# Kernel tuning notes

Hardware: AMD Instinct MI355X
Metric: run time of the kernel (lower is better)

## Reference

```python
import jax, jax.numpy as jnp
import numpy as np

BATCH, SEQ, IN, HID, LAYERS = 128, 512, 512, 1024, 2


def setup_inputs() -> dict:
    key = jax.random.key(0)
    ks = jax.random.split(key, 8)
    s = 0.02
    # Gate weights concatenated in order [forget, input, output, cell]
    W0 = jax.random.normal(ks[0], (IN + HID, 4 * HID), dtype=jnp.float32) * s
    b0 = jax.random.normal(ks[1], (4 * HID,), dtype=jnp.float32) * s
    W1 = jax.random.normal(ks[2], (HID + HID, 4 * HID), dtype=jnp.float32) * s
    b1 = jax.random.normal(ks[3], (4 * HID,), dtype=jnp.float32) * s
    Wout = jax.random.normal(ks[4], (HID, 1), dtype=jnp.float32) * s
    bout = jax.random.normal(ks[5], (1,), dtype=jnp.float32) * s
    x = jax.random.normal(ks[6], (BATCH, SEQ, IN), dtype=jnp.float32)
    return {"x": x, "W0": W0, "b0": b0, "W1": W1, "b1": b1,
            "Wout": Wout, "bout": bout}


def _cell(x_in, h_prev, c_prev, W, b):
    z = jnp.concatenate([x_in, h_prev], axis=-1) @ W + b  # (B, 4H)
    f, i, o, g = jnp.split(z, 4, axis=-1)
    c_next = jax.nn.sigmoid(f) * c_prev + jax.nn.sigmoid(i) * jnp.tanh(g)
    h_next = jax.nn.sigmoid(o) * jnp.tanh(c_next)
    return h_next, c_next


def reference(x, W0, b0, W1, b1, Wout, bout):
    B = x.shape[0]
    H = W0.shape[1] // 4
    params = ((W0, b0), (W1, b1))

    h0 = tuple(jnp.zeros((B, H), x.dtype) for _ in range(LAYERS))
    c0 = tuple(jnp.zeros((B, H), x.dtype) for _ in range(LAYERS))

    def step(carry, x_t):
        h, c = carry
        inp = x_t
        new_h, new_c = [], []
        for l in range(LAYERS):
            W, b = params[l]
            h_n, c_n = _cell(inp, h[l], c[l], W, b)
            new_h.append(h_n)
            new_c.append(c_n)
            inp = h_n
        return (tuple(new_h), tuple(new_c)), None

    xs = jnp.swapaxes(x, 0, 1)  # (T, B, IN)
    (h_fin, _), _ = jax.lax.scan(step, (h0, c0), xs)
    last = h_fin[-1]  # output of top layer at last timestep
    logits = last @ Wout + bout  # (B, 1)
    return jax.nn.sigmoid(logits).squeeze(-1)  # (B,)
```

## Files before the change

kernel.cpp:

```cpp
#include <hip/hip_runtime.h>
#include <hip/hip_bf16.h>
#include <cstdint>
#include <cstddef>


#define BATCH 128
#define SEQ   512
#define INP   512
#define HID   1024
#define NCOL  4096
#define NB    256
#define KS0   48
#define KS1   64
#define HS_   (BATCH * HID)

typedef __bf16 bf16x8 __attribute__((ext_vector_type(8)));
typedef float  f32x4  __attribute__((ext_vector_type(4)));
typedef unsigned int u32x4 __attribute__((ext_vector_type(4)));
typedef unsigned long long u64;
typedef u64 u64x2 __attribute__((ext_vector_type(2)));

__device__ __forceinline__ bf16x8 load_bf16x8(const __hip_bfloat16* p) {
    u32x4 u = *reinterpret_cast<const u32x4*>(p);
    return __builtin_bit_cast(bf16x8, u);
}
__device__ __forceinline__ bf16x8 aload_bf16x8(const __hip_bfloat16* p) {
    u64x2 q;
    q[0] = __hip_atomic_load((const u64*)p,       __ATOMIC_RELAXED, __HIP_MEMORY_SCOPE_AGENT);
    q[1] = __hip_atomic_load((const u64*)(p + 4), __ATOMIC_RELAXED, __HIP_MEMORY_SCOPE_AGENT);
    return __builtin_bit_cast(bf16x8, q);
}
__device__ __forceinline__ f32x4 mfma16(bf16x8 a, bf16x8 b, f32x4 c) {
    return __builtin_amdgcn_mfma_f32_16x16x32_bf16(a, b, c, 0, 0, 0);
}
__device__ __forceinline__ float sigmoidf_(float x) {
    return 1.0f / (1.0f + __expf(-x));
}
__device__ __forceinline__ float tanhf_(float x) {
    return 1.0f - 2.0f / (__expf(2.0f * x) + 1.0f);
}
__device__ __forceinline__ void gload16(const void* g, void* l) {
    __builtin_amdgcn_global_load_lds(
        (const __attribute__((address_space(1))) uint32_t*)g,
        (__attribute__((address_space(3))) uint32_t*)l, 16, 0, 0);
}
#define VMWAIT asm volatile("s_waitcnt vmcnt(12)" ::: "memory")

template<int Ks>
__global__ __launch_bounds__(1024)
void pack_frag_kernel(const float* __restrict__ W, __hip_bfloat16* __restrict__ F)
{
    __shared__ float tile[32][33];
    const int k0 = blockIdx.x * 32;
    const int c0 = blockIdx.y * 32;
    const int tx = threadIdx.x & 31, ty = threadIdx.x >> 5;
    tile[ty][tx] = W[(size_t)(k0 + ty) * NCOL + (c0 + tx)];
    __syncthreads();
    const int cL  = threadIdx.x >> 5;
    const int kgw = (threadIdx.x >> 3) & 3;
    const int j   = threadIdx.x & 7;
    const int c   = c0 + cL;
    const int r   = (c & 1023) * 4 + (c >> 10);
    const int nb2 = r >> 4, cl = r & 15;
    const int ks  = k0 >> 5;
    const size_t chunk = ((size_t)(nb2 * Ks + ks) * 4 + kgw) * 16 + cl;
    F[chunk * 8 + j] = __float2bfloat16(tile[kgw * 8 + j][cL]);
}

__global__ void bias_reorder_kernel(const float* __restrict__ b0,
                                    const float* __restrict__ b1,
                                    float* __restrict__ b0r,
                                    float* __restrict__ b1r)
{
    int i = blockIdx.x * blockDim.x + threadIdx.x;
    if (i >= 2 * NCOL) return;
    const float* src = (i < NCOL) ? b0 : b1;
    float*       dst = (i < NCOL) ? b0r : b1r;
    int c = i & (NCOL - 1);
    dst[(c & 1023) * 4 + (c >> 10)] = src[c];
}

__global__ __launch_bounds__(256)
void xconv_kernel(const float* __restrict__ x, __hip_bfloat16* __restrict__ xb)
{
    const int idx = blockIdx.x * 256 + threadIdx.x;
    const int r   = idx & 63;
    const int kg  = (idx >> 6) & 3;
    const int mq  = (idx >> 8) & 1;
    const int ks  = (idx >> 9) & 15;
    const int t   = idx >> 13;
    const float* src = x + ((size_t)(mq * 64 + r) * SEQ + t) * INP + ks * 32 + kg * 8;
    bf16x8 v;
    #pragma unroll
    for (int j = 0; j < 8; ++j) v[j] = (__bf16)src[j];
    *reinterpret_cast<u32x4*>(xb + (size_t)idx * 8) = __builtin_bit_cast(u32x4, v);
}

__global__ __launch_bounds__(512, 2)
void lstm_persistent(const __hip_bfloat16* __restrict__ xb,
                     const __hip_bfloat16* __restrict__ F0,
                     const __hip_bfloat16* __restrict__ F1,
                     const float* __restrict__ b0r,
                     const float* __restrict__ b1r,
                     const float* __restrict__ Wout,
                     const float* __restrict__ bout,
                     __hip_bfloat16* __restrict__ h0r,
                     __hip_bfloat16* __restrict__ h1r,
                     float* __restrict__ out,
                     int* __restrict__ bar,
                     int rm, int fm)
{
    extern __shared__ char smem[];

    __shared__ float zacc[2][128][17];
    __shared__ float cS[2][512];
    __shared__ float biasS[2][16];
    __shared__ __hip_bfloat16 hstage[2][128][4];

    const int tid  = threadIdx.x;
    const int lane = tid & 63;
    const int wv   = tid >> 6;
    const int kq   = wv & 3;
    const int mq   = wv >> 2;
    const int lm   = lane & 15;
    const int kg   = lane >> 4;
    const int nb   = blockIdx.x;
    const uint32_t sbase = (uint32_t)wv * 16384;

    bf16x8 B0r_[12], B1r_[16];
    #pragma unroll
    for (int i = 0; i < 4; ++i)
        B0r_[i]     = load_bf16x8(F0 + ((((size_t)nb * KS0 + (4*kq + i)) * 4 + kg) * 16 + lm) * 8);
    #pragma unroll
    for (int i = 0; i < 8; ++i)
        B0r_[4 + i] = load_bf16x8(F0 + ((((size_t)nb * KS0 + (16 + 8*kq + i)) * 4 + kg) * 16 + lm) * 8);
    #pragma unroll
    for (int i = 0; i < 8; ++i)
        B1r_[i]     = load_bf16x8(F1 + ((((size_t)nb * KS1 + (8*kq + i)) * 4 + kg) * 16 + lm) * 8);
    #pragma unroll
    for (int i = 0; i < 8; ++i)
        B1r_[8 + i] = load_bf16x8(F1 + ((((size_t)nb * KS1 + (32 + 8*kq + i)) * 4 + kg) * 16 + lm) * 8);
    #pragma unroll
    for (int i = 0; i < 12; ++i) asm volatile("" : "+v"(B0r_[i]));
    #pragma unroll
    for (int i = 0; i < 16; ++i) asm volatile("" : "+v"(B1r_[i]));

    if (tid < 32) biasS[tid >> 4][tid & 15] = ((tid < 16) ? b0r : b1r)[nb * 16 + (tid & 15)];
    for (int i = tid; i < 1024; i += 512) cS[i >> 9][i & 511] = 0.f;
    for (int i = tid; i < 2 * 128 * 17; i += 512) ((float*)zacc)[i] = 0.f;
    __syncthreads();

    auto issueStep = [&](const __hip_bfloat16* src, int sl) {
        const char* g = (const char*)src + (size_t)lane * 16;
        char* l = smem + sbase + (uint32_t)sl * 4096;
        #pragma unroll
        for (int i2 = 0; i2 < 4; ++i2)
            gload16(g + i2 * 1024, l + i2 * 1024);
    };
    auto readA = [&](int sl, int f) -> bf16x8 {
        const char* lp = smem + sbase + (uint32_t)sl * 4096
                       + (uint32_t)kg * 1024 + (uint32_t)f * 256 + (uint32_t)lm * 16;
        u32x4 v = *(const u32x4*)lp;
        return __builtin_bit_cast(bf16x8, v);
    };

    #pragma unroll
    for (int s = 0; s < 4; ++s)
        issueStep(xb + ((size_t)((4*kq + s) * 2 + mq)) * 2048, s);
    asm volatile("s_waitcnt vmcnt(0)" ::: "memory");

    for (int p = 0; p <= SEQ; ++p) {
        const __hip_bfloat16* h0p = h0r + (size_t)((p + rm)     & rm) * HS_;
        const __hip_bfloat16* h1p = h1r + (size_t)((p + rm - 1) & rm) * HS_;
        __hip_bfloat16*       h0w = h0r + (size_t)( p           & rm) * HS_;
        __hip_bfloat16*       h1w = h1r + (size_t)((p + rm)     & rm) * HS_;
        const int tn = (p + 1 < SEQ) ? (p + 1) : (SEQ - 1);

        f32x4 aL0[4], aL1[4];
        #pragma unroll
        for (int f = 0; f < 4; ++f) { aL0[f] = f32x4{0,0,0,0}; aL1[f] = f32x4{0,0,0,0}; }

        #pragma unroll
        for (int s = 0; s < 4; ++s) {
            bf16x8 A[4];
            #pragma unroll
            for (int f = 0; f < 4; ++f) A[f] = readA(s, f);
            #pragma unroll
            for (int f = 0; f < 4; ++f) aL0[f] = mfma16(A[f], B0r_[s], aL0[f]);
        }

        if (tid == 0) {
            const int g = nb >> 5;
            int* arrv = bar + 32 * g;
            int* root = bar + 256;
            int* rel  = bar + 512 + 32 * g;
            if ((nb & 31) == 0) {
                while (__hip_atomic_load(arrv, __ATOMIC_RELAXED, __HIP_MEMORY_SCOPE_AGENT) < 32 * p)
                    __builtin_amdgcn_s_sleep(1);
                __hip_atomic_fetch_add(root, 1, __ATOMIC_RELAXED, __HIP_MEMORY_SCOPE_AGENT);
            }
            if (nb == 0) {
                while (__hip_atomic_load(root, __ATOMIC_RELAXED, __HIP_MEMORY_SCOPE_AGENT) < 8 * (p + 1))
                    __builtin_amdgcn_s_sleep(1);
                #pragma unroll
                for (int gg = 0; gg < 8; ++gg)
                    __hip_atomic_store(bar + 512 + 32 * gg, p,
                                       __ATOMIC_RELAXED, __HIP_MEMORY_SCOPE_AGENT);
            } else {
                while (__hip_atomic_load(rel, __ATOMIC_RELAXED, __HIP_MEMORY_SCOPE_AGENT) < p)
                    __builtin_amdgcn_s_sleep(2);
            }
            if ((p & fm) == fm)
                __builtin_amdgcn_fence(__ATOMIC_ACQUIRE, "agent");
            asm volatile("" ::: "memory");
        }
        __builtin_amdgcn_s_barrier();

        #pragma unroll
        for (int s = 0; s < 4; ++s)
            issueStep(h0p + ((size_t)((8*kq + s) * 2 + mq)) * 2048, s);
        #pragma unroll
        for (int i = 0; i < 8; ++i) {
            VMWAIT;
            const int sl = (4 + i) & 3;
            bf16x8 A[4];
            #pragma unroll
            for (int f = 0; f < 4; ++f) A[f] = readA(sl, f);
            #pragma unroll
            for (int f = 0; f < 4; ++f) {
                aL0[f] = mfma16(A[f], B0r_[4 + i], aL0[f]);
                aL1[f] = mfma16(A[f], B1r_[i],     aL1[f]);
            }
            if (i < 4) issueStep(h0p + ((size_t)((8*kq + 4 + i)   * 2 + mq)) * 2048, (8 + i) & 3);
            else       issueStep(h1p + ((size_t)((8*kq + (i - 4)) * 2 + mq)) * 2048, (8 + i) & 3);
        }
        #pragma unroll
        for (int i = 0; i < 8; ++i) {
            VMWAIT;
            const int sl = (12 + i) & 3;
            bf16x8 A[4];
            #pragma unroll
            for (int f = 0; f < 4; ++f) A[f] = readA(sl, f);
            #pragma unroll
            for (int f = 0; f < 4; ++f) aL1[f] = mfma16(A[f], B1r_[8 + i], aL1[f]);
            if (i < 4)
                issueStep(h1p + ((size_t)((8*kq + 4 + i) * 2 + mq)) * 2048, (16 + i) & 3);
            else
                issueStep(xb + (size_t)tn * 65536
                             + ((size_t)((4*kq + (i - 4)) * 2 + mq)) * 2048, (16 + i) & 3);
        }

        if (p < SEQ) {
            #pragma unroll
            for (int f = 0; f < 4; ++f)
                #pragma unroll
                for (int r = 0; r < 4; ++r)
                    atomicAdd(&zacc[0][mq*64 + f*16 + kg*4 + r][lm], aL0[f][r]);
        }
        if (p >= 1) {
            #pragma unroll
            for (int f = 0; f < 4; ++f)
                #pragma unroll
                for (int r = 0; r < 4; ++r)
                    atomicAdd(&zacc[1][mq*64 + f*16 + kg*4 + r][lm], aL1[f][r]);
        }
        __syncthreads();

        for (int it = tid; it < 1024; it += 512) {
            const int L   = it >> 9;
            const int idx = it & 511;
            const int bl  = idx >> 2;
            const int u   = idx & 3;
            const bool act = L ? (p >= 1) : (p < SEQ);
            if (act) {
                float* zb = &zacc[L][bl][4 * u];
                const float zf = zb[0] + biasS[L][4*u + 0];
                const float zi = zb[1] + biasS[L][4*u + 1];
                const float zo = zb[2] + biasS[L][4*u + 2];
                const float zg = zb[3] + biasS[L][4*u + 3];
                zb[0] = 0.f; zb[1] = 0.f; zb[2] = 0.f; zb[3] = 0.f;
                const float cold = cS[L][idx];
                const float cn = sigmoidf_(zf) * cold + sigmoidf_(zi) * tanhf_(zg);
                const float hn = sigmoidf_(zo) * tanhf_(cn);
                cS[L][idx] = cn;
                hstage[L][bl][u] = __float2bfloat16(hn);
            }
        }
        __syncthreads();

        if (tid < 256) {
            const int L  = tid >> 7;
            const int bl = tid & 127;
            const bool act = L ? (p >= 1) : (p < SEQ);
            if (act) {
                __hip_bfloat16* hw = L ? h1w : h0w;
                const int uks = nb >> 3, ukg = (nb >> 1) & 3, jb = (nb & 1) * 4;
                const int mqb = bl >> 6, rr = bl & 63;
                const size_t e = ((size_t)((uks*2 + mqb)*4 + ukg)*64 + rr)*8 + jb;
                const u64 v = *(const u64*)&hstage[L][bl][0];
                __hip_atomic_store((u64*)(hw + e), v,
                                   __ATOMIC_RELAXED, __HIP_MEMORY_SCOPE_AGENT);
            }
        }
        __syncthreads();

        if (tid == 0)
            __hip_atomic_fetch_add(bar + 32 * (nb >> 5), 1,
                                   __ATOMIC_RELAXED, __HIP_MEMORY_SCOPE_AGENT);
    }

    if (nb == 0) {
        if (tid == 0) {
            #pragma unroll
            for (int gg = 0; gg < 8; ++gg)
                while (__hip_atomic_load(bar + 32 * gg, __ATOMIC_RELAXED,
                                         __HIP_MEMORY_SCOPE_AGENT) < 32 * (SEQ + 1))
                    __builtin_amdgcn_s_sleep(2);
        }
        __syncthreads();
        if (tid < BATCH) {
            const __hip_bfloat16* hb = h1r + (size_t)((SEQ - 1) & rm) * HS_;
            const int mqb = tid >> 6, rr = tid & 63;
            float acc = 0.f;
            for (int uu = 0; uu < HID; uu += 8) {
                const int uks = uu >> 5, ukg = (uu >> 3) & 3;
                const size_t e = ((size_t)((uks*2 + mqb)*4 + ukg)*64 + rr)*8;
                bf16x8 v = aload_bf16x8(hb + e);
                #pragma unroll
                for (int j = 0; j < 8; ++j) acc += (float)v[j] * Wout[uu + j];
            }
            out[tid] = 1.f / (1.f + __expf(-(acc + bout[0])));
        }
    }
}

extern "C" void kernel_launch(void* const* d_in, const int* in_sizes, int n_in,
                              void* d_out, int out_size, void* d_ws, size_t ws_size,
                              hipStream_t stream)
{
    const float* x    = (const float*)d_in[0];
    const float* W0   = (const float*)d_in[1];
    const float* b0   = (const float*)d_in[2];
    const float* W1   = (const float*)d_in[3];
    const float* b1   = (const float*)d_in[4];
    const float* Wout = (const float*)d_in[5];
    const float* bout = (const float*)d_in[6];
    float* out = (float*)d_out;

    char* ws = (char*)d_ws;
    const size_t OFF_F0  = 0;
    const size_t OFF_F1  = 12582912;
    const size_t OFF_B0R = 29360128;
    const size_t OFF_B1R = 29376512;
    const size_t OFF_BAR = 29392896;
    const size_t OFF_R0  = 29396992;
    const size_t SLOT    = 262144;
    const size_t XBYTES  = (size_t)BATCH * SEQ * INP * 2;

    int rm, fm;
    if      (ws_size >= OFF_R0 + 128 * SLOT + XBYTES) { rm = 63; fm = 31; }
    else if (ws_size >= OFF_R0 +  32 * SLOT + XBYTES) { rm = 15; fm = 7;  }
    else                                              { rm = 1;  fm = 0;  }
    const size_t OFF_R1 = OFF_R0 + (size_t)(rm + 1) * SLOT;
    const size_t OFF_XB = OFF_R1 + (size_t)(rm + 1) * SLOT;

    __hip_bfloat16* F0  = (__hip_bfloat16*)(ws + OFF_F0);
    __hip_bfloat16* F1  = (__hip_bfloat16*)(ws + OFF_F1);
    float* b0r = (float*)(ws + OFF_B0R);
    float* b1r = (float*)(ws + OFF_B1R);
    __hip_bfloat16* h0r = (__hip_bfloat16*)(ws + OFF_R0);
    __hip_bfloat16* h1r = (__hip_bfloat16*)(ws + OFF_R1);
    int* bar = (int*)(ws + OFF_BAR);
    __hip_bfloat16* xbp = (__hip_bfloat16*)(ws + OFF_XB);

    hipMemsetAsync(ws + OFF_BAR, 0, 4096, stream);
    hipMemsetAsync(ws + OFF_R0 + (size_t)rm * SLOT, 0, SLOT, stream);
    hipMemsetAsync(ws + OFF_R1 + (size_t)rm * SLOT, 0, SLOT, stream);

    pack_frag_kernel<KS0><<<dim3(48, 128), 1024, 0, stream>>>(W0, F0);
    pack_frag_kernel<KS1><<<dim3(64, 128), 1024, 0, stream>>>(W1, F1);
    bias_reorder_kernel<<<32, 256, 0, stream>>>(b0, b1, b0r, b1r);
    xconv_kernel<<<(BATCH * SEQ * INP) / (256 * 8), 256, 0, stream>>>(x, xbp);

    hipFuncSetAttribute((const void*)lstm_persistent,
                        hipFuncAttributeMaxDynamicSharedMemorySize, 131072);

    void* args[] = {(void*)&xbp, (void*)&F0, (void*)&F1, (void*)&b0r, (void*)&b1r,
                    (void*)&Wout, (void*)&bout, (void*)&h0r, (void*)&h1r,
                    (void*)&out, (void*)&bar, (void*)&rm, (void*)&fm};
    hipLaunchCooperativeKernel((void*)lstm_persistent, dim3(NB), dim3(512),
                               args, 131072, stream);
}
```

Baseline: 15.23 ms.

## Repartition LSTM blocks over batch halves and 8-unit column groups

Changes the work split so each block covers one batch half (64 rows) and 32 gate columns (8 hidden units x 4 gates). Previously each block covered all 128 batch rows and 16 columns. The weight fragments, bias order, x staging and h-state layouts are repacked so each block reads only its batch half of x and h. Each block also writes a contiguous 16-byte h chunk per row. The aim is to cut per-step global h/x traffic per block and make h stores more contiguous. In exchange each block holds more distinct weight columns, and cross-block h dependencies now span both batch halves. The register-pinning asm barriers are also removed.

```diff
diff --git a/kernel.cpp b/kernel.cpp
--- a/kernel.cpp
+++ b/kernel.cpp
@@ -12,7 +12,7 @@
 #define NB    256
 #define KS0   48
 #define KS1   64
-#define HS_   (BATCH * HID)
+#define HSLOT 131072
 
 typedef __bf16 bf16x8 __attribute__((ext_vector_type(8)));
 typedef float  f32x4  __attribute__((ext_vector_type(4)));
@@ -56,15 +56,18 @@
     const int tx = threadIdx.x & 31, ty = threadIdx.x >> 5;
     tile[ty][tx] = W[(size_t)(k0 + ty) * NCOL + (c0 + tx)];
     __syncthreads();
-    const int cL  = threadIdx.x >> 5;
-    const int kgw = (threadIdx.x >> 3) & 3;
-    const int j   = threadIdx.x & 7;
-    const int c   = c0 + cL;
-    const int r   = (c & 1023) * 4 + (c >> 10);
-    const int nb2 = r >> 4, cl = r & 15;
-    const int ks  = k0 >> 5;
-    const size_t chunk = ((size_t)(nb2 * Ks + ks) * 4 + kgw) * 16 + cl;
-    F[chunk * 8 + j] = __float2bfloat16(tile[kgw * 8 + j][cL]);
+    const int cL    = threadIdx.x >> 5;
+    const int k_off = threadIdx.x & 31;
+    const int c    = c0 + cL;
+    const int gate = c >> 10, ug = c & 1023;
+    const int ub   = ug >> 3, ul = ug & 7;
+    const int cl   = ul * 4 + gate;
+    const int cq   = cl >> 4, lm = cl & 15;
+    const int ks   = k0 >> 5;
+    const int kg   = (k_off >> 3) & 3;
+    const int j    = k_off & 7;
+    F[((((size_t)(ub * 2 + cq) * Ks + ks) * 4 + kg) * 128) + lm * 8 + j] =
+        __float2bfloat16(tile[k_off][cL]);
 }
 
 __global__ void bias_reorder_kernel(const float* __restrict__ b0,
@@ -77,23 +80,24 @@
     const float* src = (i < NCOL) ? b0 : b1;
     float*       dst = (i < NCOL) ? b0r : b1r;
     int c = i & (NCOL - 1);
-    dst[(c & 1023) * 4 + (c >> 10)] = src[c];
+    int gate = c >> 10, ug = c & 1023;
+    dst[(ug >> 3) * 32 + (ug & 7) * 4 + gate] = src[c];
 }
 
 __global__ __launch_bounds__(256)
 void xconv_kernel(const float* __restrict__ x, __hip_bfloat16* __restrict__ xb)
 {
-    const int idx = blockIdx.x * 256 + threadIdx.x;
-    const int r   = idx & 63;
-    const int kg  = (idx >> 6) & 3;
-    const int mq  = (idx >> 8) & 1;
-    const int ks  = (idx >> 9) & 15;
-    const int t   = idx >> 13;
-    const float* src = x + ((size_t)(mq * 64 + r) * SEQ + t) * INP + ks * 32 + kg * 8;
+    const int g  = blockIdx.x * 256 + threadIdx.x;
+    const int r  = g & 63;
+    const int kg = (g >> 6) & 3;
+    const int ks = (g >> 8) & 15;
+    const int m  = (g >> 12) & 1;
+    const int t  = g >> 13;
+    const float* src = x + ((size_t)(m * 64 + r) * SEQ + t) * INP + ks * 32 + kg * 8;
     bf16x8 v;
     #pragma unroll
     for (int j = 0; j < 8; ++j) v[j] = (__bf16)src[j];
-    *reinterpret_cast<u32x4*>(xb + (size_t)idx * 8) = __builtin_bit_cast(u32x4, v);
+    *reinterpret_cast<u32x4*>(xb + (size_t)g * 8) = __builtin_bit_cast(u32x4, v);
 }
 
 __global__ __launch_bounds__(512, 2)
@@ -112,42 +116,42 @@
 {
     extern __shared__ char smem[];
 
-    __shared__ float zacc[2][128][17];
+    __shared__ float zacc[2][64][33];
     __shared__ float cS[2][512];
-    __shared__ float biasS[2][16];
-    __shared__ __hip_bfloat16 hstage[2][128][4];
+    __shared__ float biasS[2][32];
+    __shared__ __hip_bfloat16 hstage[2][64][8];
 
     const int tid  = threadIdx.x;
     const int lane = tid & 63;
     const int wv   = tid >> 6;
     const int kq   = wv & 3;
-    const int mq   = wv >> 2;
+    const int cq   = wv >> 2;
     const int lm   = lane & 15;
     const int kg   = lane >> 4;
     const int nb   = blockIdx.x;
+    const int m_blk = nb & 1;
+    const int ub    = nb >> 1;
     const uint32_t sbase = (uint32_t)wv * 16384;
 
+    const __hip_bfloat16* f0b = F0 + (size_t)(ub * 2 + cq) * (KS0 * 512);
+    const __hip_bfloat16* f1b = F1 + (size_t)(ub * 2 + cq) * (KS1 * 512);
     bf16x8 B0r_[12], B1r_[16];
     #pragma unroll
     for (int i = 0; i < 4; ++i)
-        B0r_[i]     = load_bf16x8(F0 + ((((size_t)nb * KS0 + (4*kq + i)) * 4 + kg) * 16 + lm) * 8);
+        B0r_[i]     = load_bf16x8(f0b + ((size_t)(kq + 4*i) * 4 + kg) * 128 + lm * 8);
     #pragma unroll
     for (int i = 0; i < 8; ++i)
-        B0r_[4 + i] = load_bf16x8(F0 + ((((size_t)nb * KS0 + (16 + 8*kq + i)) * 4 + kg) * 16 + lm) * 8);
+        B0r_[4 + i] = load_bf16x8(f0b + ((size_t)(16 + 8*kq + i) * 4 + kg) * 128 + lm * 8);
     #pragma unroll
     for (int i = 0; i < 8; ++i)
-        B1r_[i]     = load_bf16x8(F1 + ((((size_t)nb * KS1 + (8*kq + i)) * 4 + kg) * 16 + lm) * 8);
+        B1r_[i]     = load_bf16x8(f1b + ((size_t)(8*kq + i) * 4 + kg) * 128 + lm * 8);
     #pragma unroll
     for (int i = 0; i < 8; ++i)
-        B1r_[8 + i] = load_bf16x8(F1 + ((((size_t)nb * KS1 + (32 + 8*kq + i)) * 4 + kg) * 16 + lm) * 8);
-    #pragma unroll
-    for (int i = 0; i < 12; ++i) asm volatile("" : "+v"(B0r_[i]));
-    #pragma unroll
-    for (int i = 0; i < 16; ++i) asm volatile("" : "+v"(B1r_[i]));
-
-    if (tid < 32) biasS[tid >> 4][tid & 15] = ((tid < 16) ? b0r : b1r)[nb * 16 + (tid & 15)];
+        B1r_[8 + i] = load_bf16x8(f1b + ((size_t)(32 + 8*kq + i) * 4 + kg) * 128 + lm * 8);
+
+    if (tid < 64) biasS[tid >> 5][tid & 31] = ((tid < 32) ? b0r : b1r)[ub * 32 + (tid & 31)];
     for (int i = tid; i < 1024; i += 512) cS[i >> 9][i & 511] = 0.f;
-    for (int i = tid; i < 2 * 128 * 17; i += 512) ((float*)zacc)[i] = 0.f;
+    for (int i = tid; i < 2 * 64 * 33; i += 512) ((float*)zacc)[i] = 0.f;
     __syncthreads();
 
     auto issueStep = [&](const __hip_bfloat16* src, int sl) {
@@ -166,14 +170,14 @@
 
     #pragma unroll
     for (int s = 0; s < 4; ++s)
-        issueStep(xb + ((size_t)((4*kq + s) * 2 + mq)) * 2048, s);
+        issueStep(xb + (size_t)m_blk * 32768 + (size_t)(kq + 4*s) * 2048, s);
     asm volatile("s_waitcnt vmcnt(0)" ::: "memory");
 
     for (int p = 0; p <= SEQ; ++p) {
-        const __hip_bfloat16* h0p = h0r + (size_t)((p + rm)     & rm) * HS_;
-        const __hip_bfloat16* h1p = h1r + (size_t)((p + rm - 1) & rm) * HS_;
-        __hip_bfloat16*       h0w = h0r + (size_t)( p           & rm) * HS_;
-        __hip_bfloat16*       h1w = h1r + (size_t)((p + rm)     & rm) * HS_;
+        const __hip_bfloat16* h0p = h0r + (size_t)((p + rm)     & rm) * HSLOT + (size_t)m_blk * 65536;
+        const __hip_bfloat16* h1p = h1r + (size_t)((p + rm - 1) & rm) * HSLOT + (size_t)m_blk * 65536;
+        __hip_bfloat16*       h0w = h0r + (size_t)( p           & rm) * HSLOT;
+        __hip_bfloat16*       h1w = h1r + (size_t)((p + rm)     & rm) * HSLOT;
         const int tn = (p + 1 < SEQ) ? (p + 1) : (SEQ - 1);
 
         f32x4 aL0[4], aL1[4];
@@ -218,11 +222,11 @@
 
         #pragma unroll
         for (int s = 0; s < 4; ++s)
-            issueStep(h0p + ((size_t)((8*kq + s) * 2 + mq)) * 2048, s);
+            issueStep(h0p + (size_t)(8*kq + s) * 2048, s);
         #pragma unroll
         for (int i = 0; i < 8; ++i) {
             VMWAIT;
-            const int sl = (4 + i) & 3;
+            const int sl = i & 3;
             bf16x8 A[4];
             #pragma unroll
             for (int f = 0; f < 4; ++f) A[f] = readA(sl, f);
@@ -231,23 +235,23 @@
                 aL0[f] = mfma16(A[f], B0r_[4 + i], aL0[f]);
                 aL1[f] = mfma16(A[f], B1r_[i],     aL1[f]);
             }
-            if (i < 4) issueStep(h0p + ((size_t)((8*kq + 4 + i)   * 2 + mq)) * 2048, (8 + i) & 3);
-            else       issueStep(h1p + ((size_t)((8*kq + (i - 4)) * 2 + mq)) * 2048, (8 + i) & 3);
+            if (i < 4) issueStep(h0p + (size_t)(8*kq + 4 + i) * 2048, i & 3);
+            else       issueStep(h1p + (size_t)(8*kq + (i-4)) * 2048, i & 3);
         }
         #pragma unroll
         for (int i = 0; i < 8; ++i) {
             VMWAIT;
-            const int sl = (12 + i) & 3;
+            const int sl = i & 3;
             bf16x8 A[4];
             #pragma unroll
             for (int f = 0; f < 4; ++f) A[f] = readA(sl, f);
             #pragma unroll
             for (int f = 0; f < 4; ++f) aL1[f] = mfma16(A[f], B1r_[8 + i], aL1[f]);
             if (i < 4)
-                issueStep(h1p + ((size_t)((8*kq + 4 + i) * 2 + mq)) * 2048, (16 + i) & 3);
+                issueStep(h1p + (size_t)(8*kq + 4 + i) * 2048, i & 3);
             else
-                issueStep(xb + (size_t)tn * 65536
-                             + ((size_t)((4*kq + (i - 4)) * 2 + mq)) * 2048, (16 + i) & 3);
+                issueStep(xb + (size_t)tn * 65536 + (size_t)m_blk * 32768
+                             + (size_t)(kq + 4*(i-4)) * 2048, i & 3);
         }
 
         if (p < SEQ) {
@@ -255,22 +259,22 @@
             for (int f = 0; f < 4; ++f)
                 #pragma unroll
                 for (int r = 0; r < 4; ++r)
-                    atomicAdd(&zacc[0][mq*64 + f*16 + kg*4 + r][lm], aL0[f][r]);
+                    atomicAdd(&zacc[0][f*16 + kg*4 + r][cq*16 + lm], aL0[f][r]);
         }
         if (p >= 1) {
             #pragma unroll
             for (int f = 0; f < 4; ++f)
                 #pragma unroll
                 for (int r = 0; r < 4; ++r)
-                    atomicAdd(&zacc[1][mq*64 + f*16 + kg*4 + r][lm], aL1[f][r]);
+                    atomicAdd(&zacc[1][f*16 + kg*4 + r][cq*16 + lm], aL1[f][r]);
         }
         __syncthreads();
 
         for (int it = tid; it < 1024; it += 512) {
             const int L   = it >> 9;
             const int idx = it & 511;
-            const int bl  = idx >> 2;
-            const int u   = idx & 3;
+            const int bl  = idx >> 3;
+            const int u   = idx & 7;
             const bool act = L ? (p >= 1) : (p < SEQ);
             if (act) {
                 float* zb = &zacc[L][bl][4 * u];
@@ -288,18 +292,16 @@
         }
         __syncthreads();
 
-        if (tid < 256) {
-            const int L  = tid >> 7;
-            const int bl = tid & 127;
+        if (tid < 128) {
+            const int L  = tid >> 6;
+            const int rr = tid & 63;
             const bool act = L ? (p >= 1) : (p < SEQ);
             if (act) {
-                __hip_bfloat16* hw = L ? h1w : h0w;
-                const int uks = nb >> 3, ukg = (nb >> 1) & 3, jb = (nb & 1) * 4;
-                const int mqb = bl >> 6, rr = bl & 63;
-                const size_t e = ((size_t)((uks*2 + mqb)*4 + ukg)*64 + rr)*8 + jb;
-                const u64 v = *(const u64*)&hstage[L][bl][0];
-                __hip_atomic_store((u64*)(hw + e), v,
-                                   __ATOMIC_RELAXED, __HIP_MEMORY_SCOPE_AGENT);
+                __hip_bfloat16* hw = (L ? h1w : h0w)
+                                   + (size_t)m_blk * 65536 + (size_t)ub * 512 + (size_t)rr * 8;
+                const u64* v = (const u64*)&hstage[L][rr][0];
+                __hip_atomic_store((u64*)hw,       v[0], __ATOMIC_RELAXED, __HIP_MEMORY_SCOPE_AGENT);
+                __hip_atomic_store((u64*)(hw + 4), v[1], __ATOMIC_RELAXED, __HIP_MEMORY_SCOPE_AGENT);
             }
         }
         __syncthreads();
@@ -319,15 +321,13 @@
         }
         __syncthreads();
         if (tid < BATCH) {
-            const __hip_bfloat16* hb = h1r + (size_t)((SEQ - 1) & rm) * HS_;
-            const int mqb = tid >> 6, rr = tid & 63;
+            const __hip_bfloat16* hb = h1r + (size_t)((SEQ - 1) & rm) * HSLOT
+                                     + (size_t)(tid >> 6) * 65536 + (size_t)(tid & 63) * 8;
             float acc = 0.f;
-            for (int uu = 0; uu < HID; uu += 8) {
-                const int uks = uu >> 5, ukg = (uu >> 3) & 3;
-                const size_t e = ((size_t)((uks*2 + mqb)*4 + ukg)*64 + rr)*8;
-                bf16x8 v = aload_bf16x8(hb + e);
+            for (int ub2 = 0; ub2 < 128; ++ub2) {
+                bf16x8 v = aload_bf16x8(hb + (size_t)ub2 * 512);
                 #pragma unroll
-                for (int j = 0; j < 8; ++j) acc += (float)v[j] * Wout[uu + j];
+                for (int j = 0; j < 8; ++j) acc += (float)v[j] * Wout[ub2 * 8 + j];
             }
             out[tid] = 1.f / (1.f + __expf(-(acc + bout[0])));
         }
```

Measured after the change: 15.11 ms. Within noise of the previous version (-0.7%).
